# Optimization experiments

Measured on AMD Instinct MI355X. Metric: run time of the kernel, lower is better.

## Reference

```python
import jax, jax.numpy as jnp
import numpy as np


def setup_inputs() -> dict:
    key = jax.random.key(0)
    k1, k2 = jax.random.split(key)
    B, N, M, K = 8, 4096, 4096, 64
    input1 = jax.random.normal(k1, (B, N, K), dtype=jnp.float32)
    input2 = jax.random.normal(k2, (B, M, K), dtype=jnp.float32)
    return {"input1": input1, "input2": input2}


def reference(input1, input2):
    # Pairwise L2 distances via the ||x||^2 + ||y||^2 - 2<x,y> identity,
    # avoiding the O(B*N*M*K) broadcast-subtraction intermediate.
    x2 = jnp.sum(input1 * input1, axis=-1)                 # [B, N]
    y2 = jnp.sum(input2 * input2, axis=-1)                 # [B, M]
    xy = jnp.einsum('bnk,bmk->bnm', input1, input2)        # [B, N, M]
    sq = x2[:, :, None] + y2[:, None, :] - 2.0 * xy
    D = jnp.sqrt(jnp.maximum(sq, 0.0))                     # [B, N, M]
    dist0 = jnp.mean(jnp.min(D, axis=1), axis=1)           # min over N, mean over M
    dist1 = jnp.mean(jnp.min(D, axis=2), axis=1)           # min over M, mean over N
    loss = jnp.mean(dist0 + dist1)
    return loss
```

## Files before the change

### kernel.cpp

```cpp
#include <hip/hip_runtime.h>

#define BATCH 8
#define NPTS  4096
#define KD    64
#define RS    32
#define CS    4
#define NWALK 8
#define FINF  3.0e38f

typedef float f32x4 __attribute__((ext_vector_type(4)));
typedef float f32x2 __attribute__((ext_vector_type(2)));
typedef short s16x8 __attribute__((ext_vector_type(8)));

__device__ __forceinline__ unsigned int f2bf(float f) {
  unsigned int u = __float_as_uint(f);
  u += 0x7FFFu + ((u >> 16) & 1u);
  return u >> 16;
}

__device__ __forceinline__ float min3f(float a, float b, float c) {
  return fminf(fminf(a, b), c);
}

__global__ __launch_bounds__(256)
void prep_kernel(const float* __restrict__ X, const float* __restrict__ Y,
                 unsigned int* __restrict__ Xbf, unsigned int* __restrict__ Ybf,
                 float* __restrict__ x2, float* __restrict__ y2,
                 unsigned int* __restrict__ counter) {
  int gid = blockIdx.x * 256 + threadIdx.x;
  if (gid == 0) *counter = 0;
  int row = gid >> 5;
  int ki  = gid & 31;
  bool isX = row < BATCH * NPTS;
  int r2 = row & (BATCH * NPTS - 1);
  const float* src = isX ? X : Y;
  f32x2 v = *(const f32x2*)(src + (size_t)r2 * KD + ki * 2);
  float s = v[0] * v[0] + v[1] * v[1];
  #pragma unroll
  for (int m = 16; m >= 1; m >>= 1) s += __shfl_xor(s, m, 64);
  unsigned int packed = (f2bf(v[1]) << 16) | f2bf(v[0]);
  (isX ? Xbf : Ybf)[r2 * 32 + ki] = packed;
  if (ki == 0) (isX ? x2 : y2)[r2] = s;
}

__global__ __launch_bounds__(256)
void chamfer_main(const unsigned short* __restrict__ Xbf,
                  const unsigned short* __restrict__ Ybf,
                  const float* __restrict__ x2g, const float* __restrict__ y2g,
                  float* __restrict__ rowpart,
                  float* __restrict__ colpart) {
  __shared__ float l_nm[2 * 128 * NWALK];
  __shared__ float l_cm[2 * 128];

  const int b = blockIdx.x, ms = blockIdx.y, nw = blockIdx.z;
  const int m0 = ms * 128;
  const int n0 = nw * (128 * NWALK);
  const int t = threadIdx.x, w = t >> 6, lane = t & 63, c = lane & 15, q = lane >> 4;
  const int gm = w >> 1, gn = w & 1;
  const int wm = gm * 64, wn = gn * 64;

  const unsigned short* Yg = Ybf + (size_t)(b * NPTS + m0) * KD;
  const unsigned short* Xg = Xbf + (size_t)(b * NPTS + n0) * KD;

  s16x8 yf[4][2];
  #pragma unroll
  for (int i = 0; i < 4; ++i) {
    const unsigned short* yr = Yg + (wm + i * 16 + c) * KD + q * 8;
    yf[i][0] = *(const s16x8*)yr;
    yf[i][1] = *(const s16x8*)(yr + 32);
  }
  const float* y2b = y2g + b * NPTS + m0;
  f32x4 y2r[4];
  #pragma unroll
  for (int i = 0; i < 4; ++i) y2r[i] = *(const f32x4*)(y2b + wm + i * 16 + q * 4);

  float macc[4][4];
  #pragma unroll
  for (int i = 0; i < 4; ++i)
    #pragma unroll
    for (int r = 0; r < 4; ++r) macc[i][r] = FINF;

  const float* x2b = x2g + b * NPTS + n0;
  const f32x4 zacc = {0.f, 0.f, 0.f, 0.f};

  #pragma clang loop unroll(disable)
  for (int k = 0; k < NWALK; ++k) {
    s16x8 xf[4][2];
    float x2c[4];
    #pragma unroll
    for (int j = 0; j < 4; ++j) {
      const unsigned short* xr = Xg + (k * 128 + wn + j * 16 + c) * KD + q * 8;
      xf[j][0] = *(const s16x8*)xr;
      xf[j][1] = *(const s16x8*)(xr + 32);
      x2c[j] = x2b[k * 128 + wn + j * 16 + c];
    }

    float nm[4] = {FINF, FINF, FINF, FINF};
    #pragma unroll
    for (int jp = 0; jp < 2; ++jp) {
      const int j0 = jp * 2, j1 = jp * 2 + 1;
      f32x4 acc0[4], acc1[4];
      #pragma unroll
      for (int i = 0; i < 4; ++i) {
        f32x4 a = __builtin_amdgcn_mfma_f32_16x16x32_bf16(yf[i][0], xf[j0][0], zacc, 0, 0, 0);
        acc0[i] = __builtin_amdgcn_mfma_f32_16x16x32_bf16(yf[i][1], xf[j0][1], a, 0, 0, 0);
        f32x4 bq = __builtin_amdgcn_mfma_f32_16x16x32_bf16(yf[i][0], xf[j1][0], zacc, 0, 0, 0);
        acc1[i] = __builtin_amdgcn_mfma_f32_16x16x32_bf16(yf[i][1], xf[j1][1], bq, 0, 0, 0);
      }
      #pragma unroll
      for (int i = 0; i < 4; ++i)
        #pragma unroll
        for (int rp = 0; rp < 2; ++rp) {
          const int r0 = rp * 2, r1 = rp * 2 + 1;
          float v00 = acc0[i][r0], v01 = acc0[i][r1];
          float v10 = acc1[i][r0], v11 = acc1[i][r1];
          macc[i][r0] = min3f(macc[i][r0], fmaf(-2.f, v00, x2c[j0]), fmaf(-2.f, v10, x2c[j1]));
          macc[i][r1] = min3f(macc[i][r1], fmaf(-2.f, v01, x2c[j0]), fmaf(-2.f, v11, x2c[j1]));
          nm[j0] = min3f(nm[j0], fmaf(-2.f, v00, y2r[i][r0]), fmaf(-2.f, v01, y2r[i][r1]));
          nm[j1] = min3f(nm[j1], fmaf(-2.f, v10, y2r[i][r0]), fmaf(-2.f, v11, y2r[i][r1]));
        }
    }
    #pragma unroll
    for (int j = 0; j < 4; ++j) {
      nm[j] = fminf(nm[j], __shfl_xor(nm[j], 16, 64));
      nm[j] = fminf(nm[j], __shfl_xor(nm[j], 32, 64));
    }
    float sel = (q == 0) ? nm[0] : (q == 1) ? nm[1] : (q == 2) ? nm[2] : nm[3];
    l_nm[gm * (128 * NWALK) + k * 128 + wn + q * 16 + c] = sel;
  }

  #pragma unroll
  for (int msk = 1; msk <= 8; msk <<= 1)
    #pragma unroll
    for (int i = 0; i < 4; ++i)
      #pragma unroll
      for (int r = 0; r < 4; ++r)
        macc[i][r] = fminf(macc[i][r], __shfl_xor(macc[i][r], msk, 64));
  if (c == 0) {
    #pragma unroll
    for (int i = 0; i < 4; ++i) {
      f32x4 v = {macc[i][0], macc[i][1], macc[i][2], macc[i][3]};
      *(f32x4*)&l_cm[gn * 128 + wm + i * 16 + q * 4] = v;
    }
  }
  __syncthreads();

  const size_t TOT = (size_t)BATCH * NPTS;
  float* rp_out = rowpart + (size_t)ms * TOT + b * NPTS + n0;
  #pragma unroll
  for (int u = 0; u < 4; ++u) {
    int nn = t + u * 256;
    float v = fminf(l_nm[nn], l_nm[128 * NWALK + nn]);
    rp_out[nn] = v + x2b[nn];
  }
  if (t < 128) {
    float v = fminf(l_cm[t], l_cm[128 + t]);
    colpart[(size_t)nw * TOT + b * NPTS + m0 + t] = v + y2b[t];
  }
}

__global__ __launch_bounds__(256)
void reduce_kernel(const float* __restrict__ rowpart, const float* __restrict__ colpart,
                   float* __restrict__ partials, unsigned int* __restrict__ counter,
                   float* __restrict__ out) {
  int i = blockIdx.x * 256 + threadIdx.x;
  const int TOT = BATCH * NPTS;
  float rv = FINF;
  #pragma unroll
  for (int s = 0; s < RS; ++s) rv = fminf(rv, rowpart[(size_t)s * TOT + i]);
  float s0 = sqrtf(fmaxf(rv, 0.f));
  float cv = FINF;
  #pragma unroll
  for (int s = 0; s < CS; ++s) cv = fminf(cv, colpart[(size_t)s * TOT + i]);
  s0 += sqrtf(fmaxf(cv, 0.f));
  #pragma unroll
  for (int m = 32; m >= 1; m >>= 1) s0 += __shfl_xor(s0, m, 64);
  __shared__ float wsum[4];
  if ((threadIdx.x & 63) == 0) wsum[threadIdx.x >> 6] = s0;
  __syncthreads();

  if (threadIdx.x < 64) {
    unsigned int ticket = 0;
    if (threadIdx.x == 0) {
      float bsum = wsum[0] + wsum[1] + wsum[2] + wsum[3];
      atomicExch(&partials[blockIdx.x], bsum);
      __threadfence();
      ticket = atomicAdd(counter, 1);
    }
    ticket = __shfl(ticket, 0, 64);
    if (ticket == 127) {
      float v = atomicAdd(&partials[threadIdx.x], 0.0f) +
                atomicAdd(&partials[threadIdx.x + 64], 0.0f);
      #pragma unroll
      for (int m = 32; m >= 1; m >>= 1) v += __shfl_xor(v, m, 64);
      if (threadIdx.x == 0) out[0] = v * (1.0f / (float)TOT);
    }
  }
}

extern "C" void kernel_launch(void* const* d_in, const int* in_sizes, int n_in,
                              void* d_out, int out_size, void* d_ws, size_t ws_size,
                              hipStream_t stream) {
  const float* X = (const float*)d_in[0];
  const float* Y = (const float*)d_in[1];
  float* out = (float*)d_out;

  char* ws = (char*)d_ws;
  unsigned int* Xbf = (unsigned int*)ws;
  unsigned int* Ybf = (unsigned int*)(ws + (4u << 20));
  float* x2 = (float*)(ws + (8u << 20));
  float* y2 = (float*)(ws + (8u << 20) + (128u << 10));
  float* rowpart = (float*)(ws + (8u << 20) + (256u << 10));
  float* colpart = (float*)(ws + (12u << 20) + (256u << 10));
  float* partials = (float*)(ws + (13u << 20));
  unsigned int* counter = (unsigned int*)(partials + 128);

  prep_kernel<<<dim3(2 * BATCH * NPTS * 32 / 256), dim3(256), 0, stream>>>(
      X, Y, Xbf, Ybf, x2, y2, counter);

  chamfer_main<<<dim3(BATCH, RS, CS), dim3(256), 0, stream>>>(
      (const unsigned short*)Xbf, (const unsigned short*)Ybf, x2, y2, rowpart, colpart);

  reduce_kernel<<<dim3(BATCH * NPTS / 256), dim3(256), 0, stream>>>(
      rowpart, colpart, partials, counter, out);
}
```

Measured before the change: 117.3 us.

## Double-buffer X fragments across N-walk iterations and split N into more blocks

Each block now walks 4 N-tiles instead of 8, and CS rises to 8, which doubles the grid to 2048 blocks. The loop prefetches the next tile's X bf16 fragments and norms into registers while the current tile is used for MFMAs, so global-load latency is hidden. The trade-off is more VGPRs for the double buffer and a colpart that is twice as large, so the reduce kernel makes more partial passes. The workspace offset for partials is moved to fit the bigger colpart.

Measured after the change: 123.4 us. +5.2%, slower.

```diff
diff --git a/kernel.cpp b/kernel.cpp
--- a/kernel.cpp
+++ b/kernel.cpp
@@ -4,8 +4,8 @@
 #define NPTS  4096
 #define KD    64
 #define RS    32
-#define CS    4
-#define NWALK 8
+#define CS    8
+#define NWALK 4
 #define FINF  3.0e38f
 
 typedef float f32x4 __attribute__((ext_vector_type(4)));
@@ -83,16 +83,27 @@
   const float* x2b = x2g + b * NPTS + n0;
   const f32x4 zacc = {0.f, 0.f, 0.f, 0.f};
 
+  s16x8 cur[4][2];
+  float cx2[4];
+  #pragma unroll
+  for (int j = 0; j < 4; ++j) {
+    const unsigned short* xr = Xg + (wn + j * 16 + c) * KD + q * 8;
+    cur[j][0] = *(const s16x8*)xr;
+    cur[j][1] = *(const s16x8*)(xr + 32);
+    cx2[j] = x2b[wn + j * 16 + c];
+  }
+
   #pragma clang loop unroll(disable)
   for (int k = 0; k < NWALK; ++k) {
-    s16x8 xf[4][2];
-    float x2c[4];
+    const int kn = (k + 1 < NWALK) ? k + 1 : k;
+    s16x8 nxt[4][2];
+    float nx2[4];
     #pragma unroll
     for (int j = 0; j < 4; ++j) {
-      const unsigned short* xr = Xg + (k * 128 + wn + j * 16 + c) * KD + q * 8;
-      xf[j][0] = *(const s16x8*)xr;
-      xf[j][1] = *(const s16x8*)(xr + 32);
-      x2c[j] = x2b[k * 128 + wn + j * 16 + c];
+      const unsigned short* xr = Xg + (kn * 128 + wn + j * 16 + c) * KD + q * 8;
+      nxt[j][0] = *(const s16x8*)xr;
+      nxt[j][1] = *(const s16x8*)(xr + 32);
+      nx2[j] = x2b[kn * 128 + wn + j * 16 + c];
     }
 
     float nm[4] = {FINF, FINF, FINF, FINF};
@@ -102,10 +113,10 @@
       f32x4 acc0[4], acc1[4];
       #pragma unroll
       for (int i = 0; i < 4; ++i) {
-        f32x4 a = __builtin_amdgcn_mfma_f32_16x16x32_bf16(yf[i][0], xf[j0][0], zacc, 0, 0, 0);
-        acc0[i] = __builtin_amdgcn_mfma_f32_16x16x32_bf16(yf[i][1], xf[j0][1], a, 0, 0, 0);
-        f32x4 bq = __builtin_amdgcn_mfma_f32_16x16x32_bf16(yf[i][0], xf[j1][0], zacc, 0, 0, 0);
-        acc1[i] = __builtin_amdgcn_mfma_f32_16x16x32_bf16(yf[i][1], xf[j1][1], bq, 0, 0, 0);
+        f32x4 a = __builtin_amdgcn_mfma_f32_16x16x32_bf16(yf[i][0], cur[j0][0], zacc, 0, 0, 0);
+        acc0[i] = __builtin_amdgcn_mfma_f32_16x16x32_bf16(yf[i][1], cur[j0][1], a, 0, 0, 0);
+        f32x4 bq = __builtin_amdgcn_mfma_f32_16x16x32_bf16(yf[i][0], cur[j1][0], zacc, 0, 0, 0);
+        acc1[i] = __builtin_amdgcn_mfma_f32_16x16x32_bf16(yf[i][1], cur[j1][1], bq, 0, 0, 0);
       }
       #pragma unroll
       for (int i = 0; i < 4; ++i)
@@ -114,8 +125,8 @@
           const int r0 = rp * 2, r1 = rp * 2 + 1;
           float v00 = acc0[i][r0], v01 = acc0[i][r1];
           float v10 = acc1[i][r0], v11 = acc1[i][r1];
-          macc[i][r0] = min3f(macc[i][r0], fmaf(-2.f, v00, x2c[j0]), fmaf(-2.f, v10, x2c[j1]));
-          macc[i][r1] = min3f(macc[i][r1], fmaf(-2.f, v01, x2c[j0]), fmaf(-2.f, v11, x2c[j1]));
+          macc[i][r0] = min3f(macc[i][r0], fmaf(-2.f, v00, cx2[j0]), fmaf(-2.f, v10, cx2[j1]));
+          macc[i][r1] = min3f(macc[i][r1], fmaf(-2.f, v01, cx2[j0]), fmaf(-2.f, v11, cx2[j1]));
           nm[j0] = min3f(nm[j0], fmaf(-2.f, v00, y2r[i][r0]), fmaf(-2.f, v01, y2r[i][r1]));
           nm[j1] = min3f(nm[j1], fmaf(-2.f, v10, y2r[i][r0]), fmaf(-2.f, v11, y2r[i][r1]));
         }
@@ -127,6 +138,13 @@
     }
     float sel = (q == 0) ? nm[0] : (q == 1) ? nm[1] : (q == 2) ? nm[2] : nm[3];
     l_nm[gm * (128 * NWALK) + k * 128 + wn + q * 16 + c] = sel;
+
+    #pragma unroll
+    for (int j = 0; j < 4; ++j) {
+      cur[j][0] = nxt[j][0];
+      cur[j][1] = nxt[j][1];
+      cx2[j] = nx2[j];
+    }
   }
 
   #pragma unroll
@@ -148,7 +166,7 @@
   const size_t TOT = (size_t)BATCH * NPTS;
   float* rp_out = rowpart + (size_t)ms * TOT + b * NPTS + n0;
   #pragma unroll
-  for (int u = 0; u < 4; ++u) {
+  for (int u = 0; u < 2; ++u) {
     int nn = t + u * 256;
     float v = fminf(l_nm[nn], l_nm[128 * NWALK + nn]);
     rp_out[nn] = v + x2b[nn];
@@ -212,7 +230,7 @@
   float* y2 = (float*)(ws + (8u << 20) + (128u << 10));
   float* rowpart = (float*)(ws + (8u << 20) + (256u << 10));
   float* colpart = (float*)(ws + (12u << 20) + (256u << 10));
-  float* partials = (float*)(ws + (13u << 20));
+  float* partials = (float*)(ws + (13u << 20) + (256u << 10));
   unsigned int* counter = (unsigned int*)(partials + 128);
 
   prep_kernel<<<dim3(2 * BATCH * NPTS * 32 / 256), dim3(256), 0, stream>>>(
```
